# Performance work log

Hardware: AMD Instinct MI355X
Metric: run time of the kernel (lower is better)

Reference implementation:

```python
import jax, jax.numpy as jnp
import numpy as np

N, E, FN, FE, L, G = 4096, 16384, 16, 8, 128, 64
EPS = 1e-5


def setup_inputs() -> dict:
    key = jax.random.key(0)
    ks = iter(jax.random.split(key, 40))

    def lin_w(shape):
        return jax.random.normal(next(ks), shape, jnp.float32) * (1.0 / np.sqrt(shape[0]))

    d = {}
    d["x"] = jax.random.normal(next(ks), (N, FN), jnp.float32)
    d["edge_attr"] = jax.random.normal(next(ks), (E, FE), jnp.float32)
    d["edge_index"] = jax.random.randint(next(ks), (2, E), 0, N)
    d["batch"] = jnp.sort(jax.random.randint(next(ks), (N,), 0, G))
    for i, (cin, cout) in enumerate([(FN, 32), (32, 64), (64, 128)], 1):
        d[f"We{i}"] = lin_w((FE, cin * cout))          # edge_fc weight
        d[f"be{i}"] = jnp.zeros((cin * cout,), jnp.float32)
        d[f"bias{i}"] = jnp.zeros((cout,), jnp.float32)
        d[f"Wr{i}"] = lin_w((cin, cout))               # res_fc weight
        d[f"br{i}"] = jnp.zeros((cout,), jnp.float32)
        d[f"bn_g{i}"] = jnp.ones((cout,), jnp.float32)
        d[f"bn_b{i}"] = jnp.zeros((cout,), jnp.float32)
        d[f"a{i}"] = jnp.float32(0.25)                  # PReLU slope
    d["Wi"] = lin_w((128, 128)); d["bi"] = jnp.zeros((128,), jnp.float32)
    d["Wj"] = lin_w((128, 128)); d["bj"] = jnp.zeros((128,), jnp.float32)
    d["Wfc"] = lin_w((128, 2 * L)); d["bfc"] = jnp.zeros((2 * L,), jnp.float32)
    return d


def _ecc(x, src, dst, norm, edge_attr, We, be, bias, Wr, br, cout, cin):
    # dynamically generated per-edge filter: [E, out, in]
    theta = (edge_attr @ We + be).reshape(E, cout, cin)
    # gather source features, per-edge matvec, degree-normalize (norm_j)
    msg = norm[src][:, None] * jnp.einsum('eoi,ei->eo', theta, x[src])
    # scatter-add into destination nodes + bias + residual linear
    return jax.ops.segment_sum(msg, dst, num_segments=N) + bias + x @ Wr + br


def _bn(x, g, b):
    m = x.mean(0)
    v = x.var(0)  # biased variance, as torch BN training normalization
    return (x - m) * jax.lax.rsqrt(v + EPS) * g + b


def _prelu(x, a):
    return jnp.where(x >= 0, x, a * x)


def reference(x, edge_attr, edge_index, batch,
              We1, be1, bias1, Wr1, br1, bn_g1, bn_b1, a1,
              We2, be2, bias2, Wr2, br2, bn_g2, bn_b2, a2,
              We3, be3, bias3, Wr3, br3, bn_g3, bn_b3, a3,
              Wi, bi, Wj, bj, Wfc, bfc):
    src, dst = edge_index[0], edge_index[1]
    deg = jax.ops.segment_sum(jnp.ones((E,), x.dtype), src, num_segments=N)
    norm = jnp.where(deg > 0, 1.0 / deg, 0.0)

    h = _ecc(x, src, dst, norm, edge_attr, We1, be1, bias1, Wr1, br1, 32, FN)
    h = _prelu(_bn(h, bn_g1, bn_b1), a1)
    h = _ecc(h, src, dst, norm, edge_attr, We2, be2, bias2, Wr2, br2, 64, 32)
    h = _prelu(_bn(h, bn_g2, bn_b2), a2)
    h = _ecc(h, src, dst, norm, edge_attr, We3, be3, bias3, Wr3, br3, 128, 64)
    h = _prelu(_bn(h, bn_g3, bn_b3), a3)

    # gated attention pooling (GGS-NN eq. 7), scatter-sum per graph
    gates = jax.nn.sigmoid(h @ Wi + bi)
    feats = jnp.tanh(h @ Wj + bj)
    pooled = jnp.tanh(jax.ops.segment_sum(gates * feats, batch, num_segments=G))

    z = pooled @ Wfc + bfc  # [G, 2L]
    return z[:, :L], z[:, L:]
```

## Files before the change

kernel.cpp:

```cpp
#include <hip/hip_runtime.h>
#include <math.h>

#define NN 4096
#define NE 16384
#define NG 64

#define OFF_DEG   0
#define OFF_H1    4096
#define OFF_H2    135168
#define OFF_H3    397312
#define OFF_ST1   921600
#define OFF_ST2   921664
#define OFF_ST3   921792
#define OFF_POOL  922048
#define OFF_WC1   930240
#define OFF_WC2   934848
#define OFF_WC3   953280
#define OFF_Y     1027008
#define ZERO_FLOATS 930240

__device__ __forceinline__ void tr_wcat(const float* We, const float* be,
                                        float* Wcat, int CIN, int COUT, int t) {
    int nine = 9 * COUT;
    int i = t / nine; int r = t - i * nine;
    int f = r / COUT; int o = r - f * COUT;
    Wcat[t] = (f < 8) ? We[f * CIN * COUT + o * CIN + i] : be[o * CIN + i];
}

__global__ __launch_bounds__(256) void k_prep(
    const float* __restrict__ We1, const float* __restrict__ be1,
    const float* __restrict__ We2, const float* __restrict__ be2,
    const float* __restrict__ We3, const float* __restrict__ be3,
    const int* __restrict__ ei, float* __restrict__ ws)
{
    int t = blockIdx.x * 256 + threadIdx.x;
    if (t < 4608)  { tr_wcat(We1, be1, ws + OFF_WC1, 16, 32, t); return; }
    t -= 4608;
    if (t < 18432) { tr_wcat(We2, be2, ws + OFF_WC2, 32, 64, t); return; }
    t -= 18432;
    if (t < 73728) { tr_wcat(We3, be3, ws + OFF_WC3, 64, 128, t); return; }
    t -= 73728;
    if (t < NE)    { atomicAdd(&ws[OFF_DEG + ei[t]], 1.0f); }
}

template<int K, bool BN>
__global__ __launch_bounds__(256) void k_proj(
    const float* __restrict__ A,
    const float* __restrict__ B,
    const float* __restrict__ deg,
    float* __restrict__ Y, int Ncols,
    const float* __restrict__ st, const float* __restrict__ g,
    const float* __restrict__ b, const float* __restrict__ a)
{
    __shared__ float sA[K][68];
    __shared__ float sB[K][68];
    __shared__ float sS[K];
    __shared__ float sT[K];
    __shared__ float sAl;
    const int tid = threadIdx.x;
    const int m0 = blockIdx.x * 64;
    const int n0 = blockIdx.y * 64;

    if constexpr (BN) {
        if (tid < K) {
            float mean = st[tid] * (1.f / NN);
            float var  = st[K + tid] * (1.f / NN) - mean * mean;
            var = fmaxf(var, 0.f);
            float inv = rsqrtf(var + 1e-5f);
            float s = inv * g[tid];
            sS[tid] = s;
            sT[tid] = b[tid] - mean * s;
        }
        if (tid == 0) sAl = a[0];
    }
    __syncthreads();
    float al = 0.f;
    if constexpr (BN) al = sAl;

    for (int t = tid; t < 64 * K; t += 256) {
        int m = t / K, i = t - m * K;
        float v = A[(m0 + m) * K + i];
        if constexpr (BN) {
            v = fmaf(v, sS[i], sT[i]);
            v = v >= 0.f ? v : al * v;
        }
        sA[i][m] = v;
    }
    for (int t = tid; t < 64 * K; t += 256) {
        int i = t / 64, n = t - i * 64;
        int col = n0 + n;
        sB[i][n] = (col < Ncols) ? B[i * Ncols + col] : 0.f;
    }
    __syncthreads();

    const int tn = tid % 16, tm = tid / 16;
    float acc[4][4] = {{0.f}};
#pragma unroll 8
    for (int i = 0; i < K; ++i) {
        float4 av = *(const float4*)&sA[i][tm * 4];
        float4 bv = *(const float4*)&sB[i][tn * 4];
        acc[0][0] += av.x * bv.x; acc[0][1] += av.x * bv.y; acc[0][2] += av.x * bv.z; acc[0][3] += av.x * bv.w;
        acc[1][0] += av.y * bv.x; acc[1][1] += av.y * bv.y; acc[1][2] += av.y * bv.z; acc[1][3] += av.y * bv.w;
        acc[2][0] += av.z * bv.x; acc[2][1] += av.z * bv.y; acc[2][2] += av.z * bv.z; acc[2][3] += av.z * bv.w;
        acc[3][0] += av.w * bv.x; acc[3][1] += av.w * bv.y; acc[3][2] += av.w * bv.z; acc[3][3] += av.w * bv.w;
    }

#pragma unroll
    for (int mm = 0; mm < 4; ++mm) {
        int m = m0 + tm * 4 + mm;
        float d = deg[m];
        float nrm = d > 0.f ? 1.f / d : 0.f;
#pragma unroll
        for (int nn = 0; nn < 4; ++nn) {
            int col = n0 + tn * 4 + nn;
            if (col < Ncols) Y[(size_t)m * Ncols + col] = acc[mm][nn] * nrm;
        }
    }
}

template<int COUT>
__global__ __launch_bounds__(256) void k_egather(
    const float* __restrict__ Y, const float* __restrict__ eattr,
    const int* __restrict__ ei, float* __restrict__ h)
{
    constexpr int TPE = COUT / 4;
    int idx = blockIdx.x * 256 + threadIdx.x;
    int e = idx / TPE;
    int q = idx - e * TPE;
    int src = ei[e], dst = ei[NE + e];
    const float4* y4 = (const float4*)(Y + (size_t)src * (9 * COUT));
    const float4* ea4 = (const float4*)(eattr + e * 8);
    float4 ea0 = ea4[0], ea1 = ea4[1];
    float4 acc = y4[8 * TPE + q];
#define FMA4(s, v) { float4 _t = (v); acc.x += (s)*_t.x; acc.y += (s)*_t.y; acc.z += (s)*_t.z; acc.w += (s)*_t.w; }
    FMA4(ea0.x, y4[0 * TPE + q]);
    FMA4(ea0.y, y4[1 * TPE + q]);
    FMA4(ea0.z, y4[2 * TPE + q]);
    FMA4(ea0.w, y4[3 * TPE + q]);
    FMA4(ea1.x, y4[4 * TPE + q]);
    FMA4(ea1.y, y4[5 * TPE + q]);
    FMA4(ea1.z, y4[6 * TPE + q]);
    FMA4(ea1.w, y4[7 * TPE + q]);
#undef FMA4
    float* hp = h + (size_t)dst * COUT + 4 * q;
    atomicAdd(hp + 0, acc.x);
    atomicAdd(hp + 1, acc.y);
    atomicAdd(hp + 2, acc.z);
    atomicAdd(hp + 3, acc.w);
}

template<int CIN, int COUT, int KN, bool BN>
__global__ __launch_bounds__(256) void k_node(
    const float* __restrict__ xin, const float* __restrict__ Wr,
    const float* __restrict__ br, const float* __restrict__ bias,
    float* __restrict__ h, float* __restrict__ st_out,
    const float* __restrict__ st_in, const float* __restrict__ g,
    const float* __restrict__ b, const float* __restrict__ a)
{
    constexpr int NL = 256 / COUT;
    constexpr int NB = NL * KN;
    constexpr int CINP = CIN | 1;
    __shared__ float sWr[CIN * COUT];
    __shared__ float sX[NB * CINP];
    __shared__ float sred[256];
    __shared__ float sS[CIN];
    __shared__ float sT[CIN];
    __shared__ float sAl;
    const int tid = threadIdx.x;
    const int nbase = blockIdx.x * NB;

    if constexpr (BN) {
        if (tid < CIN) {
            float mean = st_in[tid] * (1.f / NN);
            float var  = st_in[CIN + tid] * (1.f / NN) - mean * mean;
            var = fmaxf(var, 0.f);
            float inv = rsqrtf(var + 1e-5f);
            float s = inv * g[tid];
            sS[tid] = s;
            sT[tid] = b[tid] - mean * s;
        }
        if (tid == 0) sAl = a[0];
    }
    for (int t = tid; t < CIN * COUT; t += 256) sWr[t] = Wr[t];
    __syncthreads();
    float al = 0.f;
    if constexpr (BN) al = sAl;

    for (int t = tid; t < NB * CIN; t += 256) {
        int r = t / CIN, i = t - r * CIN;
        float v = xin[(nbase + r) * CIN + i];
        if constexpr (BN) {
            v = fmaf(v, sS[i], sT[i]);
            v = v >= 0.f ? v : al * v;
        }
        sX[r * CINP + i] = v;
    }
    __syncthreads();

    const int o = tid % COUT;
    const int nl = tid / COUT;
    const float addc = bias[o] + br[o];
    float sum = 0.f, sumsq = 0.f;
    for (int k = 0; k < KN; ++k) {
        int r = nl * KN + k;
        float acc = addc;
        for (int i = 0; i < CIN; ++i)
            acc += sX[r * CINP + i] * sWr[i * COUT + o];
        int gi = (nbase + r) * COUT + o;
        float hv = h[gi] + acc;
        h[gi] = hv;
        sum += hv; sumsq += hv * hv;
    }
    sred[tid] = sum;
    __syncthreads();
    if (tid < COUT) {
        float s = 0.f;
        for (int g2 = 0; g2 < NL; ++g2) s += sred[g2 * COUT + tid];
        atomicAdd(&st_out[tid], s);
    }
    __syncthreads();
    sred[tid] = sumsq;
    __syncthreads();
    if (tid < COUT) {
        float s = 0.f;
        for (int g2 = 0; g2 < NL; ++g2) s += sred[g2 * COUT + tid];
        atomicAdd(&st_out[COUT + tid], s);
    }
}

__global__ __launch_bounds__(256) void k_pool(
    const float* __restrict__ h3, const int* __restrict__ batch,
    const float* __restrict__ Wi, const float* __restrict__ bi,
    const float* __restrict__ Wj, const float* __restrict__ bj,
    float* __restrict__ pooled,
    const float* __restrict__ st, const float* __restrict__ g,
    const float* __restrict__ b, const float* __restrict__ a)
{
    constexpr int KN = 8, NB = 16;
    __shared__ float sH[NB * 128];
    __shared__ int sB[NB];
    __shared__ float sS[128];
    __shared__ float sT[128];
    __shared__ float sAl;
    const int tid = threadIdx.x;
    const int nbase = blockIdx.x * NB;

    if (tid < 128) {
        float mean = st[tid] * (1.f / NN);
        float var  = st[128 + tid] * (1.f / NN) - mean * mean;
        var = fmaxf(var, 0.f);
        float inv = rsqrtf(var + 1e-5f);
        float s = inv * g[tid];
        sS[tid] = s;
        sT[tid] = b[tid] - mean * s;
    }
    if (tid == 0) sAl = a[0];
    __syncthreads();
    const float al = sAl;

    for (int t = tid; t < NB * 128; t += 256) {
        int c = t & 127;
        float v = h3[nbase * 128 + t];
        v = fmaf(v, sS[c], sT[c]);
        v = v >= 0.f ? v : al * v;
        sH[t] = v;
    }
    if (tid < NB) sB[tid] = batch[nbase + tid];
    __syncthreads();

    const int o = tid % 128, nl = tid / 128;
    float gacc[KN], facc[KN];
#pragma unroll
    for (int k = 0; k < KN; ++k) { gacc[k] = 0.f; facc[k] = 0.f; }
    for (int i = 0; i < 128; ++i) {
        float wi = Wi[i * 128 + o], wj = Wj[i * 128 + o];
#pragma unroll
        for (int k = 0; k < KN; ++k) {
            float hv = sH[(nl * KN + k) * 128 + i];
            gacc[k] += hv * wi;
            facc[k] += hv * wj;
        }
    }
    float bio = bi[o], bjo = bj[o];
#pragma unroll
    for (int k = 0; k < KN; ++k) {
        int r = nl * KN + k;
        float gate = 1.f / (1.f + expf(-(gacc[k] + bio)));
        float feat = tanhf(facc[k] + bjo);
        atomicAdd(&pooled[sB[r] * 128 + o], gate * feat);
    }
}

__global__ __launch_bounds__(256) void k_final(
    const float* __restrict__ pooled, const float* __restrict__ Wfc,
    const float* __restrict__ bfc, float* __restrict__ out)
{
    __shared__ float sP[128];
    const int g = blockIdx.x, c = threadIdx.x;
    if (c < 128) sP[c] = tanhf(pooled[g * 128 + c]);
    __syncthreads();
    float z = bfc[c];
    for (int i = 0; i < 128; ++i) z += sP[i] * Wfc[i * 256 + c];
    int oidx = (c < 128) ? (g * 128 + c) : (NG * 128 + g * 128 + (c - 128));
    out[oidx] = z;
}

extern "C" void kernel_launch(void* const* d_in, const int* in_sizes, int n_in,
                              void* d_out, int out_size, void* d_ws, size_t ws_size,
                              hipStream_t stream)
{
    (void)in_sizes; (void)n_in; (void)out_size; (void)ws_size;
    const float* x     = (const float*)d_in[0];
    const float* eattr = (const float*)d_in[1];
    const int*   ei    = (const int*)d_in[2];
    const int*   batch = (const int*)d_in[3];
    const float* We1 = (const float*)d_in[4];
    const float* be1 = (const float*)d_in[5];
    const float* bias1 = (const float*)d_in[6];
    const float* Wr1 = (const float*)d_in[7];
    const float* br1 = (const float*)d_in[8];
    const float* bg1 = (const float*)d_in[9];
    const float* bb1 = (const float*)d_in[10];
    const float* a1  = (const float*)d_in[11];
    const float* We2 = (const float*)d_in[12];
    const float* be2 = (const float*)d_in[13];
    const float* bias2 = (const float*)d_in[14];
    const float* Wr2 = (const float*)d_in[15];
    const float* br2 = (const float*)d_in[16];
    const float* bg2 = (const float*)d_in[17];
    const float* bb2 = (const float*)d_in[18];
    const float* a2  = (const float*)d_in[19];
    const float* We3 = (const float*)d_in[20];
    const float* be3 = (const float*)d_in[21];
    const float* bias3 = (const float*)d_in[22];
    const float* Wr3 = (const float*)d_in[23];
    const float* br3 = (const float*)d_in[24];
    const float* bg3 = (const float*)d_in[25];
    const float* bb3 = (const float*)d_in[26];
    const float* a3  = (const float*)d_in[27];
    const float* Wi  = (const float*)d_in[28];
    const float* bi  = (const float*)d_in[29];
    const float* Wj  = (const float*)d_in[30];
    const float* bj  = (const float*)d_in[31];
    const float* Wfc = (const float*)d_in[32];
    const float* bfc = (const float*)d_in[33];
    float* ws  = (float*)d_ws;
    float* out = (float*)d_out;

    hipMemsetAsync(d_ws, 0, (size_t)ZERO_FLOATS * sizeof(float), stream);
    k_prep<<<442, 256, 0, stream>>>(We1, be1, We2, be2, We3, be3, ei, ws);

    k_proj<16, false><<<dim3(64, 5), 256, 0, stream>>>(
        x, ws + OFF_WC1, ws + OFF_DEG, ws + OFF_Y, 288,
        nullptr, nullptr, nullptr, nullptr);
    k_egather<32><<<NE * 8 / 256, 256, 0, stream>>>(ws + OFF_Y, eattr, ei, ws + OFF_H1);
    k_node<16, 32, 2, false><<<NN / 16, 256, 0, stream>>>(
        x, Wr1, br1, bias1, ws + OFF_H1, ws + OFF_ST1,
        nullptr, nullptr, nullptr, nullptr);

    k_proj<32, true><<<dim3(64, 9), 256, 0, stream>>>(
        ws + OFF_H1, ws + OFF_WC2, ws + OFF_DEG, ws + OFF_Y, 576,
        ws + OFF_ST1, bg1, bb1, a1);
    k_egather<64><<<NE * 16 / 256, 256, 0, stream>>>(ws + OFF_Y, eattr, ei, ws + OFF_H2);
    k_node<32, 64, 4, true><<<NN / 16, 256, 0, stream>>>(
        ws + OFF_H1, Wr2, br2, bias2, ws + OFF_H2, ws + OFF_ST2,
        ws + OFF_ST1, bg1, bb1, a1);

    k_proj<64, true><<<dim3(64, 18), 256, 0, stream>>>(
        ws + OFF_H2, ws + OFF_WC3, ws + OFF_DEG, ws + OFF_Y, 1152,
        ws + OFF_ST2, bg2, bb2, a2);
    k_egather<128><<<NE * 32 / 256, 256, 0, stream>>>(ws + OFF_Y, eattr, ei, ws + OFF_H3);
    k_node<64, 128, 8, true><<<NN / 16, 256, 0, stream>>>(
        ws + OFF_H2, Wr3, br3, bias3, ws + OFF_H3, ws + OFF_ST3,
        ws + OFF_ST2, bg2, bb2, a2);

    k_pool<<<NN / 16, 256, 0, stream>>>(ws + OFF_H3, batch, Wi, bi, Wj, bj, ws + OFF_POOL,
                                        ws + OFF_ST3, bg3, bb3, a3);
    k_final<<<NG, 256, 0, stream>>>(ws + OFF_POOL, Wfc, bfc, out);
}
```

Baseline: 295.5 us.

## Replace atomic edge scatter with CSR gather fused into node kernel

Builds a destination-sorted CSR (counts in prep, single-block scan and fill) so each node pulls its incoming edge messages instead of edges atomically scattering into h. The gather is fused into the node kernel alongside the residual linear and BN statistics, which removes three edge kernels, the float atomics and the large memset of the h buffers. In exchange it adds a serial one-block scan kernel and per-node loops whose trip count varies with degree, so load imbalance is possible. The summation order also becomes deterministic.

After: 329.6 us. 1.12x slower.

```diff
diff --git a/kernel.cpp b/kernel.cpp
--- a/kernel.cpp
+++ b/kernel.cpp
@@ -5,19 +5,22 @@
 #define NE 16384
 #define NG 64
 
-#define OFF_DEG   0
-#define OFF_H1    4096
-#define OFF_H2    135168
-#define OFF_H3    397312
-#define OFF_ST1   921600
-#define OFF_ST2   921664
-#define OFF_ST3   921792
-#define OFF_POOL  922048
-#define OFF_WC1   930240
-#define OFF_WC2   934848
-#define OFF_WC3   953280
-#define OFF_Y     1027008
-#define ZERO_FLOATS 930240
+#define OFF_DEG    0
+#define OFF_CNT    4096
+#define OFF_ST1    8192
+#define OFF_ST2    8256
+#define OFF_ST3    8384
+#define OFF_POOL   8640
+#define ZERO_FLOATS 16832
+#define OFF_ROW    16832
+#define OFF_ELIST  20992
+#define OFF_WC1    37376
+#define OFF_WC2    41984
+#define OFF_WC3    60416
+#define OFF_H1     134144
+#define OFF_H2     265216
+#define OFF_H3     527360
+#define OFF_Y      1051648
 
 __device__ __forceinline__ void tr_wcat(const float* We, const float* be,
                                         float* Wcat, int CIN, int COUT, int t) {
@@ -40,15 +43,50 @@
     t -= 18432;
     if (t < 73728) { tr_wcat(We3, be3, ws + OFF_WC3, 64, 128, t); return; }
     t -= 73728;
-    if (t < NE)    { atomicAdd(&ws[OFF_DEG + ei[t]], 1.0f); }
+    if (t < NE) {
+        atomicAdd(&ws[OFF_DEG + ei[t]], 1.0f);
+        atomicAdd(&((int*)(ws + OFF_CNT))[ei[NE + t]], 1);
+    }
+}
+
+__global__ __launch_bounds__(1024) void k_scan(const int* __restrict__ ei,
+                                               float* __restrict__ ws)
+{
+    __shared__ int s[1024];
+    int* cnt    = (int*)(ws + OFF_CNT);
+    int* rowptr = (int*)(ws + OFF_ROW);
+    int* elist  = (int*)(ws + OFF_ELIST);
+    const int tid = threadIdx.x;
+
+    int4 c = ((const int4*)cnt)[tid];
+    int mysum = c.x + c.y + c.z + c.w;
+    s[tid] = mysum;
+    __syncthreads();
+    for (int off = 1; off < 1024; off <<= 1) {
+        int v = (tid >= off) ? s[tid - off] : 0;
+        __syncthreads();
+        s[tid] += v;
+        __syncthreads();
+    }
+    int base = s[tid] - mysum;
+    rowptr[4 * tid + 0] = base;
+    rowptr[4 * tid + 1] = base + c.x;
+    rowptr[4 * tid + 2] = base + c.x + c.y;
+    rowptr[4 * tid + 3] = base + c.x + c.y + c.z;
+    if (tid == 1023) rowptr[4096] = s[1023];
+    ((int4*)cnt)[tid] = make_int4(0, 0, 0, 0);
+    __syncthreads();
+    for (int e = tid; e < NE; e += 1024) {
+        int dst = ei[NE + e];
+        int pos = rowptr[dst] + atomicAdd(&cnt[dst], 1);
+        elist[pos] = (ei[e] << 14) | e;
+    }
 }
 
 template<int K, bool BN>
 __global__ __launch_bounds__(256) void k_proj(
-    const float* __restrict__ A,
-    const float* __restrict__ B,
-    const float* __restrict__ deg,
-    float* __restrict__ Y, int Ncols,
+    const float* __restrict__ A, const float* __restrict__ Bm,
+    const float* __restrict__ deg, float* __restrict__ Y, int Ncols,
     const float* __restrict__ st, const float* __restrict__ g,
     const float* __restrict__ b, const float* __restrict__ a)
 {
@@ -56,26 +94,23 @@
     __shared__ float sB[K][68];
     __shared__ float sS[K];
     __shared__ float sT[K];
-    __shared__ float sAl;
     const int tid = threadIdx.x;
     const int m0 = blockIdx.x * 64;
     const int n0 = blockIdx.y * 64;
 
+    float al = 0.f;
     if constexpr (BN) {
         if (tid < K) {
             float mean = st[tid] * (1.f / NN);
             float var  = st[K + tid] * (1.f / NN) - mean * mean;
             var = fmaxf(var, 0.f);
-            float inv = rsqrtf(var + 1e-5f);
-            float s = inv * g[tid];
+            float s = rsqrtf(var + 1e-5f) * g[tid];
             sS[tid] = s;
             sT[tid] = b[tid] - mean * s;
         }
-        if (tid == 0) sAl = a[0];
-    }
-    __syncthreads();
-    float al = 0.f;
-    if constexpr (BN) al = sAl;
+        al = a[0];
+        __syncthreads();
+    }
 
     for (int t = tid; t < 64 * K; t += 256) {
         int m = t / K, i = t - m * K;
@@ -87,13 +122,13 @@
         sA[i][m] = v;
     }
     for (int t = tid; t < 64 * K; t += 256) {
-        int i = t / 64, n = t - i * 64;
+        int i = t >> 6, n = t & 63;
         int col = n0 + n;
-        sB[i][n] = (col < Ncols) ? B[i * Ncols + col] : 0.f;
-    }
-    __syncthreads();
-
-    const int tn = tid % 16, tm = tid / 16;
+        sB[i][n] = (col < Ncols) ? Bm[i * Ncols + col] : 0.f;
+    }
+    __syncthreads();
+
+    const int tn = tid & 15, tm = tid >> 4;
     float acc[4][4] = {{0.f}};
 #pragma unroll 8
     for (int i = 0; i < K; ++i) {
@@ -118,54 +153,24 @@
     }
 }
 
-template<int COUT>
-__global__ __launch_bounds__(256) void k_egather(
-    const float* __restrict__ Y, const float* __restrict__ eattr,
-    const int* __restrict__ ei, float* __restrict__ h)
-{
-    constexpr int TPE = COUT / 4;
-    int idx = blockIdx.x * 256 + threadIdx.x;
-    int e = idx / TPE;
-    int q = idx - e * TPE;
-    int src = ei[e], dst = ei[NE + e];
-    const float4* y4 = (const float4*)(Y + (size_t)src * (9 * COUT));
-    const float4* ea4 = (const float4*)(eattr + e * 8);
-    float4 ea0 = ea4[0], ea1 = ea4[1];
-    float4 acc = y4[8 * TPE + q];
-#define FMA4(s, v) { float4 _t = (v); acc.x += (s)*_t.x; acc.y += (s)*_t.y; acc.z += (s)*_t.z; acc.w += (s)*_t.w; }
-    FMA4(ea0.x, y4[0 * TPE + q]);
-    FMA4(ea0.y, y4[1 * TPE + q]);
-    FMA4(ea0.z, y4[2 * TPE + q]);
-    FMA4(ea0.w, y4[3 * TPE + q]);
-    FMA4(ea1.x, y4[4 * TPE + q]);
-    FMA4(ea1.y, y4[5 * TPE + q]);
-    FMA4(ea1.z, y4[6 * TPE + q]);
-    FMA4(ea1.w, y4[7 * TPE + q]);
-#undef FMA4
-    float* hp = h + (size_t)dst * COUT + 4 * q;
-    atomicAdd(hp + 0, acc.x);
-    atomicAdd(hp + 1, acc.y);
-    atomicAdd(hp + 2, acc.z);
-    atomicAdd(hp + 3, acc.w);
-}
-
-template<int CIN, int COUT, int KN, bool BN>
-__global__ __launch_bounds__(256) void k_node(
+template<int CIN, int COUT, int NB, bool BN>
+__global__ __launch_bounds__(256) void k_gnode(
     const float* __restrict__ xin, const float* __restrict__ Wr,
     const float* __restrict__ br, const float* __restrict__ bias,
+    const float* __restrict__ Y, const float* __restrict__ eattr,
+    const int* __restrict__ rowptr, const int* __restrict__ elist,
     float* __restrict__ h, float* __restrict__ st_out,
     const float* __restrict__ st_in, const float* __restrict__ g,
     const float* __restrict__ b, const float* __restrict__ a)
 {
     constexpr int NL = 256 / COUT;
-    constexpr int NB = NL * KN;
+    constexpr int KN = NB / NL;
     constexpr int CINP = CIN | 1;
     __shared__ float sWr[CIN * COUT];
     __shared__ float sX[NB * CINP];
     __shared__ float sred[256];
     __shared__ float sS[CIN];
     __shared__ float sT[CIN];
-    __shared__ float sAl;
     const int tid = threadIdx.x;
     const int nbase = blockIdx.x * NB;
 
@@ -174,17 +179,15 @@
             float mean = st_in[tid] * (1.f / NN);
             float var  = st_in[CIN + tid] * (1.f / NN) - mean * mean;
             var = fmaxf(var, 0.f);
-            float inv = rsqrtf(var + 1e-5f);
-            float s = inv * g[tid];
+            float s = rsqrtf(var + 1e-5f) * g[tid];
             sS[tid] = s;
             sT[tid] = b[tid] - mean * s;
         }
-        if (tid == 0) sAl = a[0];
     }
     for (int t = tid; t < CIN * COUT; t += 256) sWr[t] = Wr[t];
     __syncthreads();
     float al = 0.f;
-    if constexpr (BN) al = sAl;
+    if constexpr (BN) al = a[0];
 
     for (int t = tid; t < NB * CIN; t += 256) {
         int r = t / CIN, i = t - r * CIN;
@@ -201,21 +204,33 @@
     const int nl = tid / COUT;
     const float addc = bias[o] + br[o];
     float sum = 0.f, sumsq = 0.f;
+#pragma unroll
     for (int k = 0; k < KN; ++k) {
         int r = nl * KN + k;
+        int gn = nbase + r;
         float acc = addc;
         for (int i = 0; i < CIN; ++i)
             acc += sX[r * CINP + i] * sWr[i * COUT + o];
-        int gi = (nbase + r) * COUT + o;
-        float hv = h[gi] + acc;
-        h[gi] = hv;
-        sum += hv; sumsq += hv * hv;
+        int e0 = rowptr[gn], e1 = rowptr[gn + 1];
+        for (int j = e0; j < e1; ++j) {
+            int pk = elist[j];
+            int src = pk >> 14;
+            int e = pk & 16383;
+            const float* y = Y + (size_t)src * (9 * COUT);
+            const float* ea = eattr + e * 8;
+            float m = y[8 * COUT + o];
+#pragma unroll
+            for (int f = 0; f < 8; ++f) m += ea[f] * y[f * COUT + o];
+            acc += m;
+        }
+        h[gn * COUT + o] = acc;
+        sum += acc; sumsq += acc * acc;
     }
     sred[tid] = sum;
     __syncthreads();
     if (tid < COUT) {
         float s = 0.f;
-        for (int g2 = 0; g2 < NL; ++g2) s += sred[g2 * COUT + tid];
+        for (int q = 0; q < NL; ++q) s += sred[q * COUT + tid];
         atomicAdd(&st_out[tid], s);
     }
     __syncthreads();
@@ -223,7 +238,7 @@
     __syncthreads();
     if (tid < COUT) {
         float s = 0.f;
-        for (int g2 = 0; g2 < NL; ++g2) s += sred[g2 * COUT + tid];
+        for (int q = 0; q < NL; ++q) s += sred[q * COUT + tid];
         atomicAdd(&st_out[COUT + tid], s);
     }
 }
@@ -241,7 +256,6 @@
     __shared__ int sB[NB];
     __shared__ float sS[128];
     __shared__ float sT[128];
-    __shared__ float sAl;
     const int tid = threadIdx.x;
     const int nbase = blockIdx.x * NB;
 
@@ -249,14 +263,13 @@
         float mean = st[tid] * (1.f / NN);
         float var  = st[128 + tid] * (1.f / NN) - mean * mean;
         var = fmaxf(var, 0.f);
-        float inv = rsqrtf(var + 1e-5f);
-        float s = inv * g[tid];
+        float s = rsqrtf(var + 1e-5f) * g[tid];
         sS[tid] = s;
         sT[tid] = b[tid] - mean * s;
     }
-    if (tid == 0) sAl = a[0];
-    __syncthreads();
-    const float al = sAl;
+    if (tid < NB) sB[tid] = batch[nbase + tid];
+    __syncthreads();
+    const float al = a[0];
 
     for (int t = tid; t < NB * 128; t += 256) {
         int c = t & 127;
@@ -265,10 +278,9 @@
         v = v >= 0.f ? v : al * v;
         sH[t] = v;
     }
-    if (tid < NB) sB[tid] = batch[nbase + tid];
-    __syncthreads();
-
-    const int o = tid % 128, nl = tid / 128;
+    __syncthreads();
+
+    const int o = tid & 127, nl = tid >> 7;
     float gacc[KN], facc[KN];
 #pragma unroll
     for (int k = 0; k < KN; ++k) { gacc[k] = 0.f; facc[k] = 0.f; }
@@ -346,33 +358,33 @@
     const float* bfc = (const float*)d_in[33];
     float* ws  = (float*)d_ws;
     float* out = (float*)d_out;
+    const int* rowptr = (const int*)(ws + OFF_ROW);
+    const int* elist  = (const int*)(ws + OFF_ELIST);
 
     hipMemsetAsync(d_ws, 0, (size_t)ZERO_FLOATS * sizeof(float), stream);
-    k_prep<<<442, 256, 0, stream>>>(We1, be1, We2, be2, We3, be3, ei, ws);
+    k_prep<<<506, 256, 0, stream>>>(We1, be1, We2, be2, We3, be3, ei, ws);
+    k_scan<<<1, 1024, 0, stream>>>(ei, ws);
 
     k_proj<16, false><<<dim3(64, 5), 256, 0, stream>>>(
         x, ws + OFF_WC1, ws + OFF_DEG, ws + OFF_Y, 288,
         nullptr, nullptr, nullptr, nullptr);
-    k_egather<32><<<NE * 8 / 256, 256, 0, stream>>>(ws + OFF_Y, eattr, ei, ws + OFF_H1);
-    k_node<16, 32, 2, false><<<NN / 16, 256, 0, stream>>>(
-        x, Wr1, br1, bias1, ws + OFF_H1, ws + OFF_ST1,
-        nullptr, nullptr, nullptr, nullptr);
+    k_gnode<16, 32, 8, false><<<NN / 8, 256, 0, stream>>>(
+        x, Wr1, br1, bias1, ws + OFF_Y, eattr, rowptr, elist,
+        ws + OFF_H1, ws + OFF_ST1, nullptr, nullptr, nullptr, nullptr);
 
     k_proj<32, true><<<dim3(64, 9), 256, 0, stream>>>(
         ws + OFF_H1, ws + OFF_WC2, ws + OFF_DEG, ws + OFF_Y, 576,
         ws + OFF_ST1, bg1, bb1, a1);
-    k_egather<64><<<NE * 16 / 256, 256, 0, stream>>>(ws + OFF_Y, eattr, ei, ws + OFF_H2);
-    k_node<32, 64, 4, true><<<NN / 16, 256, 0, stream>>>(
-        ws + OFF_H1, Wr2, br2, bias2, ws + OFF_H2, ws + OFF_ST2,
-        ws + OFF_ST1, bg1, bb1, a1);
+    k_gnode<32, 64, 8, true><<<NN / 8, 256, 0, stream>>>(
+        ws + OFF_H1, Wr2, br2, bias2, ws + OFF_Y, eattr, rowptr, elist,
+        ws + OFF_H2, ws + OFF_ST2, ws + OFF_ST1, bg1, bb1, a1);
 
     k_proj<64, true><<<dim3(64, 18), 256, 0, stream>>>(
         ws + OFF_H2, ws + OFF_WC3, ws + OFF_DEG, ws + OFF_Y, 1152,
         ws + OFF_ST2, bg2, bb2, a2);
-    k_egather<128><<<NE * 32 / 256, 256, 0, stream>>>(ws + OFF_Y, eattr, ei, ws + OFF_H3);
-    k_node<64, 128, 8, true><<<NN / 16, 256, 0, stream>>>(
-        ws + OFF_H2, Wr3, br3, bias3, ws + OFF_H3, ws + OFF_ST3,
-        ws + OFF_ST2, bg2, bb2, a2);
+    k_gnode<64, 128, 8, true><<<NN / 8, 256, 0, stream>>>(
+        ws + OFF_H2, Wr3, br3, bias3, ws + OFF_Y, eattr, rowptr, elist,
+        ws + OFF_H3, ws + OFF_ST3, ws + OFF_ST2, bg2, bb2, a2);
 
     k_pool<<<NN / 16, 256, 0, stream>>>(ws + OFF_H3, batch, Wi, bi, Wj, bj, ws + OFF_POOL,
                                         ws + OFF_ST3, bg3, bb3, a3);
```
